# Optimization experiments

Measured on AMD Instinct MI355X. Metric: run time of the kernel, lower is better.

Reference implementation:

```python
import jax, jax.numpy as jnp
import numpy as np

B, N, K, D, H, W = 16, 32, 32, 64, 128, 128  # batch, instances, dot_number, dot_dimension, fmap HxW
IMAGE_SIZE = 512.0
DOWN = 4.0
HID = 128


def setup_inputs() -> dict:
    key = jax.random.key(0)
    ks = jax.random.split(key, 16)
    s = 0.05
    x = jax.random.normal(ks[0], (B, 64, H, W), jnp.float32)
    mask_point = jax.random.uniform(ks[1], (B, N, K, 2), jnp.float32) * 511.0  # image-space coords
    point_mask = jnp.ones((B, N, K), jnp.int32)  # 1 = real point, 0 = zero-padded
    return {
        "x": x,
        "mask_point": mask_point,
        "point_mask": point_mask,
        "conv1_w": jax.random.normal(ks[2], (64, 64, 3, 3), jnp.float32) * s,
        "conv1_b": jnp.zeros((64,), jnp.float32),
        "conv2_w": jax.random.normal(ks[3], (D, 64), jnp.float32) * s,
        "conv2_b": jnp.full((D,), -2.19, jnp.float32),  # bias_fill with bias_value
        "Wih_e": jax.random.normal(ks[4], (4 * HID, D), jnp.float32) * s,
        "Whh_e": jax.random.normal(ks[5], (4 * HID, HID), jnp.float32) * s,
        "bih_e": jnp.zeros((4 * HID,), jnp.float32),
        "bhh_e": jnp.zeros((4 * HID,), jnp.float32),
        "Wih_d": jax.random.normal(ks[6], (4 * HID, HID), jnp.float32) * s,
        "Whh_d": jax.random.normal(ks[7], (4 * HID, HID), jnp.float32) * s,
        "bih_d": jnp.zeros((4 * HID,), jnp.float32),
        "bhh_d": jnp.zeros((4 * HID,), jnp.float32),
        "W1": jax.random.normal(ks[8], (64, HID), jnp.float32) * s,
        "b1": jnp.zeros((64,), jnp.float32),
        "W2": jax.random.normal(ks[9], (2, 64), jnp.float32) * s,
        "b2": jnp.zeros((2,), jnp.float32),
    }


def _lstm(seq, Wih, Whh, bih, bhh, h0, c0):
    # seq: [T, Bflat, in]; PyTorch gate order i, f, g, o
    bias = bih + bhh
    def step(carry, xt):
        h, c = carry
        g = xt @ Wih.T + h @ Whh.T + bias
        i, f, gg, o = jnp.split(g, 4, axis=-1)
        c = jax.nn.sigmoid(f) * c + jax.nn.sigmoid(i) * jnp.tanh(gg)
        h = jax.nn.sigmoid(o) * jnp.tanh(c)
        return (h, c), h
    (hT, cT), ys = jax.lax.scan(step, (h0, c0), seq)
    return ys, (hT, cT)


def reference(x, mask_point, point_mask, conv1_w, conv1_b, conv2_w, conv2_b,
              Wih_e, Whh_e, bih_e, bhh_e, Wih_d, Whh_d, bih_d, bhh_d,
              W1, b1, W2, b2):
    # SingleHead extraction: 3x3 conv -> ReLU -> 1x1 conv
    feat = jax.lax.conv_general_dilated(
        x, conv1_w, (1, 1), 'SAME',
        dimension_numbers=('NCHW', 'OIHW', 'NCHW')) + conv1_b[None, :, None, None]
    feat = jax.nn.relu(feat)
    fmap = jnp.einsum('bchw,dc->bdhw', feat, conv2_w) + conv2_b[None, :, None, None]
    xf = fmap.reshape(B, D, H * W)

    # keypoint index math (vectorized version of the nested python loops)
    pts = jnp.minimum(mask_point / DOWN, 127.0)        # [B,N,K,2] feature-map coords
    gt = pts * DOWN                                     # gt_keypoints
    flat = (pts[..., 1] * (IMAGE_SIZE / DOWN) + pts[..., 0]).astype(jnp.int32)  # [B,N,K]

    # gather dot features; zero padding where point_mask == 0
    dots = jax.vmap(lambda f, idx: f.T[idx])(xf, flat)  # [B,N,K,D]
    dots = dots * point_mask[..., None].astype(dots.dtype)

    seq = dots.reshape(B * N, K, D).transpose(1, 0, 2)  # [K, B*N, D] (time-major)
    h0 = jnp.zeros((B * N, HID), seq.dtype)
    enc, (h, c) = _lstm(seq, Wih_e, Whh_e, bih_e, bhh_e, h0, h0)
    dec, _ = _lstm(enc, Wih_d, Whh_d, bih_d, bhh_d, h, c)

    y = jax.nn.relu(dec @ W1.T + b1) @ W2.T + b2        # [K, B*N, 2]
    kp = y.transpose(1, 0, 2).reshape(B, N, K, 2)
    return kp, gt
```

## Files before the change

kernel.cpp:

```cpp
#include <hip/hip_runtime.h>
#include <stdint.h>

#define NSEQ 512
#define HIDN 128

#define OFF_FEIH   0
#define OFF_BIAS_E 65536
#define OFF_BIAS_D 67584
#define OFF_W1P    69632
#define OFF_W2P    143360
#define OFF_FLAT   151552
#define OFF_W1H    217088
#define OFF_FEHH   233472
#define OFF_FDIH8  364544
#define OFF_FDHH8  430080
#define OFF_W2T    495616
#define OFF_DOTS   (1024*1024)
#define OFF_XT     (4*1024*1024)
#define WS_NEED_XT ((size_t)(4*1024*1024) + (size_t)16*128*128*64*2 + 1024)

typedef _Float16 h2f __attribute__((ext_vector_type(2)));
typedef _Float16 f16x8 __attribute__((ext_vector_type(8)));
typedef float    f32x4 __attribute__((ext_vector_type(4)));

static __device__ __forceinline__ h2f u2h(uint32_t u) {
  union { uint32_t u; h2f h; } v; v.u = u; return v.h;
}

#if __has_builtin(__builtin_amdgcn_fdot2)
static __device__ __forceinline__ float fdot2_(uint32_t a, uint32_t b, float c) {
  return __builtin_amdgcn_fdot2(u2h(a), u2h(b), c, false);
}
#else
static __device__ __forceinline__ float fdot2_(uint32_t a, uint32_t b, float c) {
  h2f x = u2h(a), y = u2h(b);
  return c + (float)x.x * (float)y.x + (float)x.y * (float)y.y;
}
#endif

static __device__ __forceinline__ uint32_t packh(float a, float b) {
  union { _Float16 h[2]; uint32_t u; } v;
  v.h[0] = (_Float16)a; v.h[1] = (_Float16)b; return v.u;
}
static __device__ __forceinline__ float sig_(float x) {
  return 1.0f / (1.0f + __expf(-x));
}
static __device__ __forceinline__ float tanh_(float x) {
  return 1.0f - 2.0f / (1.0f + __expf(2.0f * x));
}

static __device__ __forceinline__ uint32_t f2e4m3_sw(float f) {
  union { float f; uint32_t u; } v; v.f = f;
  uint32_t s = (v.u >> 24) & 0x80u;
  float af = fabsf(f);
  if (af == 0.0f) return s;
  if (af >= 448.0f) return s | 0x7Eu;
  int e; float m = frexpf(af, &e);
  int E = e + 6;
  float mant = m * 2.0f - 1.0f;
  int mm = (int)(mant * 8.0f + 0.5f);
  if (mm == 8) { mm = 0; ++E; }
  if (E < 1) {
    int sm = (int)(af * 512.0f + 0.5f);
    return s | (uint32_t)(sm > 7 ? 7 : sm);
  }
  if (E > 15) return s | 0x7Eu;
  return s | ((uint32_t)E << 3) | (uint32_t)mm;
}
static __device__ __forceinline__ uint32_t pk4_fp8(float a, float b, float c, float d) {
#if __has_builtin(__builtin_amdgcn_cvt_pk_fp8_f32)
  int r = __builtin_amdgcn_cvt_pk_fp8_f32(a, b, 0, false);
  r = __builtin_amdgcn_cvt_pk_fp8_f32(c, d, r, true);
  return (uint32_t)r;
#else
  return f2e4m3_sw(a) | (f2e4m3_sw(b) << 8) | (f2e4m3_sw(c) << 16) | (f2e4m3_sw(d) << 24);
#endif
}
static __device__ __forceinline__ uint8_t f8_(float v) {
#if __has_builtin(__builtin_amdgcn_cvt_pk_fp8_f32)
  return (uint8_t)(__builtin_amdgcn_cvt_pk_fp8_f32(v, 0.f, 0, false) & 0xFF);
#else
  return (uint8_t)f2e4m3_sw(v);
#endif
}
static __device__ __forceinline__ long u2l(uint2 v) {
  union { uint2 v; long l; } x; x.v = v; return x.l;
}
static __device__ __forceinline__ uint2 ldg_frag8(const uint2* p) {
  uint2 r;
  asm volatile("global_load_dwordx2 %0, %1, off" : "=v"(r) : "v"(p));
  return r;
}
static __device__ __forceinline__ void frag_fence() {
  asm volatile("s_waitcnt vmcnt(0)" ::: "memory");
  __builtin_amdgcn_sched_barrier(0);
}

__global__ __launch_bounds__(256) void prep_kernel(
    const float* Wih_e, const float* Whh_e,
    const float* bih_e, const float* bhh_e,
    const float* Wih_d, const float* Whh_d,
    const float* bih_d, const float* bhh_d,
    const float* w1, const float* w2, const float* W1,
    const float* mask_point, float* out_gt, int* flat,
    char* ws, int w1_order) {
  float*    bias_e = (float*)(ws + OFF_BIAS_E);
  float*    bias_d = (float*)(ws + OFF_BIAS_D);
  uint32_t* w1p    = (uint32_t*)(ws + OFF_W1P);
  uint32_t* w2p    = (uint32_t*)(ws + OFF_W2P);
  uint32_t* W1h    = (uint32_t*)(ws + OFF_W1H);
  uint32_t* w2t    = (uint32_t*)(ws + OFF_W2T);

  int idx = blockIdx.x * 256 + threadIdx.x;
  if (idx < 16384) {
    int j2 = idx & 3, lane = (idx >> 2) & 63, kt = (idx >> 8) & 1, gt = idx >> 9;
    int g = gt*16 + (lane & 15);
    int k = kt*32 + ((lane >> 4) & 3)*8 + 2*j2;
    ((uint32_t*)(ws + OFF_FEIH))[idx] = packh(Wih_e[g*64 + k], Wih_e[g*64 + k + 1]);
    return;
  }
  idx -= 16384;
  if (idx < 512) { bias_e[idx] = bih_e[idx] + bhh_e[idx]; return; }
  idx -= 512;
  if (idx < 512) { bias_d[idx] = bih_d[idx] + bhh_d[idx]; return; }
  idx -= 512;
  if (idx < 288*64) {
    int i2 = idx >> 6, c = idx & 63;
    if (w1_order) {
      int tap = i2 >> 5, cin = (i2 & 31) * 2;
      w1p[idx] = packh(w1[c*576 + cin*9 + tap], w1[c*576 + (cin+1)*9 + tap]);
    } else {
      w1p[idx] = packh(w1[c*576 + 2*i2], w1[c*576 + 2*i2 + 1]);
    }
    return;
  }
  idx -= 288*64;
  if (idx < 32*64) {
    int c2 = idx >> 6, d = idx & 63;
    w2p[idx] = packh(w2[d*64 + 2*c2], w2[d*64 + 2*c2 + 1]);
    return;
  }
  idx -= 32*64;
  if (idx < 64*64) {
    int k2 = idx >> 6, j = idx & 63;
    W1h[idx] = packh(W1[j*128 + 2*k2], W1[j*128 + 2*k2 + 1]);
    return;
  }
  idx -= 64*64;
  if (idx < 32768) {
    int j2 = idx & 3, lane = (idx >> 2) & 63, kt = (idx >> 8) & 3, gt = idx >> 10;
    int g = gt*16 + (lane & 15);
    int k = kt*32 + ((lane >> 4) & 3)*8 + 2*j2;
    ((uint32_t*)(ws + OFF_FEHH))[idx] = packh(Whh_e[g*128 + k], Whh_e[g*128 + k + 1]);
    return;
  }
  idx -= 32768;
  if (idx < 16384) {
    int half = idx & 1, lane = (idx >> 1) & 63, kt = (idx >> 7) & 3, gt = idx >> 9;
    int g = gt*16 + (lane & 15);
    int kb = kt*32 + ((lane >> 4) & 3)*8 + half*4;
    const float* W = Wih_d;
    ((uint32_t*)(ws + OFF_FDIH8))[(((gt*4 + kt)*64 + lane) << 1) | half] =
        pk4_fp8(W[g*128 + kb], W[g*128 + kb + 1], W[g*128 + kb + 2], W[g*128 + kb + 3]);
    return;
  }
  idx -= 16384;
  if (idx < 16384) {
    int half = idx & 1, lane = (idx >> 1) & 63, kt = (idx >> 7) & 3, gt = idx >> 9;
    int g = gt*16 + (lane & 15);
    int kb = kt*32 + ((lane >> 4) & 3)*8 + half*4;
    const float* W = Whh_d;
    ((uint32_t*)(ws + OFF_FDHH8))[(((gt*4 + kt)*64 + lane) << 1) | half] =
        pk4_fp8(W[g*128 + kb], W[g*128 + kb + 1], W[g*128 + kb + 2], W[g*128 + kb + 3]);
    return;
  }
  idx -= 16384;
  if (idx < 64*36) {
    int d = idx / 36, c2 = idx - (idx/36)*36;
    w2t[idx] = (c2 < 32) ? packh(w2[d*64 + 2*c2], w2[d*64 + 2*c2 + 1]) : 0u;
    return;
  }
  idx -= 64*36;
  if (idx < 16384) {
    float mx = mask_point[idx*2 + 0];
    float my = mask_point[idx*2 + 1];
    float fx = fminf(mx * 0.25f, 127.0f);
    float fy = fminf(my * 0.25f, 127.0f);
    out_gt[idx*2 + 0] = fx * 4.0f;
    out_gt[idx*2 + 1] = fy * 4.0f;
    flat[idx] = (int)(__fmaf_rn(fy, 128.0f, fx));
    return;
  }
}
#define PREP_TOTAL (16384 + 512 + 512 + 288*64 + 32*64 + 64*64 + 32768 + 16384 + 16384 + 64*36 + 16384)

__global__ __launch_bounds__(256, 2) void transpose_kernel(
    const float* x, uint32_t* xT32) {
  __shared__ float lds[64][257];
  int bid = blockIdx.x;
  int xt = bid & 3, yt = (bid >> 2) & 15, b = bid >> 6;
  int x0 = xt * 32, y0 = yt * 8;
  int tx = threadIdx.x & 31, ty = threadIdx.x >> 5;
  #pragma unroll 8
  for (int c = 0; c < 64; ++c)
    lds[c][ty*32 + tx] = x[((b*64 + c)*128 + (y0 + ty))*128 + (x0 + tx)];
  __syncthreads();
  #pragma unroll 8
  for (int r = 0; r < 32; ++r) {
    int i = threadIdx.x + 256*r;
    int c2 = i & 31, pos = i >> 5;
    int yy = pos >> 5, xx = pos & 31;
    float lo = lds[2*c2][yy*32 + xx], hi = lds[2*c2 + 1][yy*32 + xx];
    xT32[((b*128 + y0 + yy)*128 + (x0 + xx))*32 + c2] = packh(lo, hi);
  }
}

__global__ __launch_bounds__(512, 1) void conv_mfma_kernel(
    const uint32_t* xT32, const int* point_mask,
    const float* conv1_b, const float* conv2_b,
    const char* ws_ro, _Float16* dots_h, const int* flat) {
  __shared__ __attribute__((aligned(16))) uint32_t w1s[64*292];
  __shared__ __attribute__((aligned(16))) uint32_t patch2[32*292];
  __shared__ __attribute__((aligned(16))) uint32_t t1s[32*36];

  const uint32_t* w1p = (const uint32_t*)(ws_ro + OFF_W1P);
  const uint32_t* w2t = (const uint32_t*)(ws_ro + OFF_W2T);
  int tid  = threadIdx.x;
  int lane = tid & 63, wave = tid >> 6;
  int r = wave & 3, g = wave >> 2;
  int cl = lane & 15, lgrp = lane >> 4;

  for (int i = tid; i < 288*64; i += 512) {
    int i2 = i >> 6, cc = i & 63;
    w1s[cc*292 + i2] = w1p[i];
  }

  uint4 a2[2];
  #pragma unroll
  for (int kt = 0; kt < 2; ++kt)
    a2[kt] = *(const uint4*)&w2t[(r*16 + cl)*36 + kt*16 + lgrp*4];

  float4 b1v = *(const float4*)&conv1_b[r*16 + lgrp*4];
  float4 b2v = *(const float4*)&conv2_b[r*16 + lgrp*4];

  for (int it = 0; it < 2; ++it) {
    int p0 = blockIdx.x * 64 + it * 32;
    __syncthreads();
    #pragma unroll
    for (int rr = 0; rr < 18; ++rr) {
      int u = tid + 512*rr;
      int slot = u / 288, w = u - slot*288;
      int tap = w >> 5, c2i = w & 31;
      int p = p0 + slot;
      int fl = flat[p];
      int hh = fl >> 7, ww = fl & 127;
      int b = p >> 10;
      int dy = tap / 3, dx = tap - dy*3;
      int yy = hh + dy - 1, xx = ww + dx - 1;
      uint32_t v = 0u;
      if (yy >= 0 && yy < 128 && xx >= 0 && xx < 128)
        v = xT32[((b*128 + yy)*128 + xx)*32 + c2i];
      patch2[slot*292 + w] = v;
    }
    __syncthreads();

    f32x4 acc = {b1v.x, b1v.y, b1v.z, b1v.w};
    #pragma unroll
    for (int kt = 0; kt < 18; ++kt) {
      f16x8 af = *(const f16x8*)&w1s[(r*16 + cl)*292 + kt*16 + lgrp*4];
      f16x8 bf = *(const f16x8*)&patch2[(g*16 + cl)*292 + kt*16 + lgrp*4];
      acc = __builtin_amdgcn_mfma_f32_16x16x32_f16(af, bf, acc, 0, 0, 0);
    }
    {
      int trow = (g*16 + cl)*36 + r*8 + lgrp*2;
      t1s[trow]     = packh(fmaxf(acc[0], 0.f), fmaxf(acc[1], 0.f));
      t1s[trow + 1] = packh(fmaxf(acc[2], 0.f), fmaxf(acc[3], 0.f));
    }
    __syncthreads();

    f32x4 acc2 = {b2v.x, b2v.y, b2v.z, b2v.w};
    #pragma unroll
    for (int kt = 0; kt < 2; ++kt) {
      f16x8 af; __builtin_memcpy(&af, &a2[kt], 16);
      f16x8 bf = *(const f16x8*)&t1s[(g*16 + cl)*36 + kt*16 + lgrp*4];
      acc2 = __builtin_amdgcn_mfma_f32_16x16x32_f16(af, bf, acc2, 0, 0, 0);
    }
    {
      int p = p0 + g*16 + cl;
      float m = (float)point_mask[p];
      int kk = p & 31, bn = p >> 5;
      int d0 = r*16 + lgrp*4;
      uint2 o;
      o.x = packh(acc2[0]*m, acc2[1]*m);
      o.y = packh(acc2[2]*m, acc2[3]*m);
      *(uint2*)&dots_h[(size_t)(kk*NSEQ + bn)*64 + d0] = o;
    }
  }
}

__global__ __launch_bounds__(256, 2) void conv_gather_kernel(
    const float* x, const int* point_mask,
    const float* conv1_b, const float* conv2_b,
    const char* ws_ro, _Float16* dots_h, const int* flat) {
  __shared__ uint32_t w1s[64*292];
  __shared__ uint32_t patch2[4*288];
  __shared__ uint32_t tl2[4*32];

  const uint32_t* w1p = (const uint32_t*)(ws_ro + OFF_W1P);
  const uint32_t* w2p = (const uint32_t*)(ws_ro + OFF_W2P);
  int tid = threadIdx.x;
  for (int i = tid; i < 288*64; i += 256) {
    int i2 = i >> 6, cc = i & 63;
    w1s[cc*292 + i2] = w1p[i];
  }

  int q = tid >> 6, c = tid & 63;
  float c1b = conv1_b[c], c2b = conv2_b[c];

  for (int g = 0; g < 8; ++g) {
    int p0 = blockIdx.x * 32 + g * 4;
    __syncthreads();
    #pragma unroll
    for (int r = 0; r < 9; ++r) {
      int l = tid + 256*r;
      int slot = l / 576;
      int within = l - slot*576;
      int cp = within / 9;
      int tap = within - cp*9;
      int p = p0 + slot;
      int fl = flat[p];
      int hh = fl >> 7, ww = fl & 127;
      int b = p >> 10;
      int yy = hh + tap/3 - 1, xx = ww + tap%3 - 1;
      float v = 0.0f;
      if (yy >= 0 && yy < 128 && xx >= 0 && xx < 128)
        v = x[((b*64 + cp)*128 + yy)*128 + xx];
      ((_Float16*)patch2)[l] = (_Float16)v;
    }
    __syncthreads();

    float a0 = c1b, a1 = 0.f, a2 = 0.f, a3 = 0.f;
    int cbase = c * 292, pbase = q * 288;
    #pragma unroll 4
    for (int i2 = 0; i2 < 288; i2 += 4) {
      a0 = fdot2_(w1s[cbase + i2+0], patch2[pbase + i2+0], a0);
      a1 = fdot2_(w1s[cbase + i2+1], patch2[pbase + i2+1], a1);
      a2 = fdot2_(w1s[cbase + i2+2], patch2[pbase + i2+2], a2);
      a3 = fdot2_(w1s[cbase + i2+3], patch2[pbase + i2+3], a3);
    }
    float t1 = fmaxf((a0 + a1) + (a2 + a3), 0.0f);
    ((_Float16*)tl2)[q*64 + c] = (_Float16)t1;

    float acc2 = c2b;
    #pragma unroll
    for (int c2i = 0; c2i < 32; ++c2i)
      acc2 = fdot2_(w2p[c2i*64 + c], tl2[q*32 + c2i], acc2);
    int p = p0 + q;
    acc2 *= (float)point_mask[p];
    int k = p & 31, bn = p >> 5;
    dots_h[(k*NSEQ + bn)*64 + c] = (_Float16)acc2;
  }
}

__global__ __launch_bounds__(512, 2) void lstm_head_kernel(
    const char* ws_ro,
    const float* b1, const float* W2, const float* b2,
    float* out_kp) {
  const f16x8* feih   = (const f16x8*)(ws_ro + OFF_FEIH);
  const f16x8* fehh   = (const f16x8*)(ws_ro + OFF_FEHH);
  const uint2* fdih8  = (const uint2*)(ws_ro + OFF_FDIH8);
  const uint2* fdhh8  = (const uint2*)(ws_ro + OFF_FDHH8);
  const float* bias_e = (const float*)(ws_ro + OFF_BIAS_E);
  const float* bias_d = (const float*)(ws_ro + OFF_BIAS_D);
  const uint32_t* dots_u = (const uint32_t*)(ws_ro + OFF_DOTS);
  const uint32_t* W1h = (const uint32_t*)(ws_ro + OFF_W1H);

  __shared__ __attribute__((aligned(16))) uint32_t xs[2][32][32];
  __shared__ __attribute__((aligned(16))) uint32_t enc8[2][32][32];
  __shared__ __attribute__((aligned(16))) uint32_t dech2[2][32][64];
  __shared__ __attribute__((aligned(16))) uint32_t hb2[2][64];
  __shared__ __attribute__((aligned(16))) uint32_t hb8[2][32];
  __shared__ __attribute__((aligned(16))) float    gb[2][512];
  __shared__ float hidf[64][65];

  int tid  = threadIdx.x;
  int lane = tid & 63, wave = tid >> 6;
  int col  = lane & 15, lgrp = lane >> 4;
  int sb   = col & 1;
  int bn0  = blockIdx.x * 2;

  int s_nl = tid >> 7, u_nl = tid & 127;
  float c_reg = 0.0f;

  for (int i = tid; i < 2048; i += 512) {
    int s = i >> 10, rem = i & 1023, t = rem >> 5, k2 = rem & 31;
    xs[s][t][k2] = dots_u[(t*NSEQ + bn0 + s)*32 + k2];
  }

  f16x8 ax[4][2], ae[4][4];
  #pragma unroll
  for (int g0 = 0; g0 < 4; ++g0) {
    #pragma unroll
    for (int kt = 0; kt < 2; ++kt)
      ax[g0][kt] = feih[((wave*4 + g0)*2 + kt)*64 + lane];
    #pragma unroll
    for (int kt = 0; kt < 4; ++kt)
      ae[g0][kt] = fehh[((wave*4 + g0)*4 + kt)*64 + lane];
  }

  float be0 = bias_e[u_nl],       be1 = bias_e[128 + u_nl];
  float be2 = bias_e[256 + u_nl], be3 = bias_e[384 + u_nl];

  if (tid < 128) hb2[tid >> 6][tid & 63] = 0u;
  __syncthreads();

  const f16x8 bzero = {};

  for (int t = 0; t < 32; ++t) {
    f16x8 bx[2], bf[4];
    #pragma unroll
    for (int kt = 0; kt < 2; ++kt)
      bx[kt] = *(const f16x8*)&xs[sb][t][kt*16 + lgrp*4];
    #pragma unroll
    for (int kt = 0; kt < 4; ++kt) {
      if (col < 2) bf[kt] = *(const f16x8*)&hb2[col][kt*16 + lgrp*4];
      else         bf[kt] = bzero;
    }
    #pragma unroll
    for (int g0 = 0; g0 < 4; ++g0) {
      f32x4 acc = {0.f, 0.f, 0.f, 0.f};
      #pragma unroll
      for (int kt = 0; kt < 2; ++kt)
        acc = __builtin_amdgcn_mfma_f32_16x16x32_f16(ax[g0][kt], bx[kt], acc, 0, 0, 0);
      #pragma unroll
      for (int kt = 0; kt < 4; ++kt)
        acc = __builtin_amdgcn_mfma_f32_16x16x32_f16(ae[g0][kt], bf[kt], acc, 0, 0, 0);
      if (col < 2)
        *(f32x4*)&gb[col][(wave*4 + g0)*16 + lgrp*4] = acc;
    }
    __syncthreads();
    if (tid < 256) {
      float ig = sig_ (gb[s_nl][u_nl]       + be0);
      float fg = sig_ (gb[s_nl][128 + u_nl] + be1);
      float gg = tanh_(gb[s_nl][256 + u_nl] + be2);
      float og = sig_ (gb[s_nl][384 + u_nl] + be3);
      c_reg = fg * c_reg + ig * gg;
      float hh = og * tanh_(c_reg);
      ((_Float16*)&hb2[s_nl][0])[u_nl] = (_Float16)hh;
      ((uint8_t*)&enc8[s_nl][t][0])[u_nl] = f8_(hh);
    }
    __syncthreads();
  }

  if (tid < 256) {
    float hv = (float)((_Float16*)&hb2[s_nl][0])[u_nl];
    ((uint8_t*)&hb8[s_nl][0])[u_nl] = f8_(hv);
  }

  uint2 dih8[4][4], dhh8[4][4];
  #pragma unroll
  for (int g0 = 0; g0 < 4; ++g0)
    #pragma unroll
    for (int kt = 0; kt < 4; ++kt) {
      dih8[g0][kt] = ldg_frag8(&fdih8[((wave*4 + g0)*4 + kt)*64 + lane]);
      dhh8[g0][kt] = ldg_frag8(&fdhh8[((wave*4 + g0)*4 + kt)*64 + lane]);
    }
  frag_fence();
  float bdi = 0.f, bdf = 0.f, bdg = 0.f, bdo = 0.f;
  if (tid < 256) {
    bdi = bias_d[u_nl];       bdf = bias_d[128 + u_nl];
    bdg = bias_d[256 + u_nl]; bdo = bias_d[384 + u_nl];
  }
  __syncthreads();

  for (int t = 0; t < 32; ++t) {
    long bx[4], bh[4];
    #pragma unroll
    for (int kt = 0; kt < 4; ++kt) {
      if (col < 2) {
        bx[kt] = u2l(*(const uint2*)&enc8[col][t][kt*8 + lgrp*2]);
        bh[kt] = u2l(*(const uint2*)&hb8[col][kt*8 + lgrp*2]);
      } else { bx[kt] = 0; bh[kt] = 0; }
    }
    #pragma unroll
    for (int g0 = 0; g0 < 4; ++g0) {
      f32x4 acc = {0.f, 0.f, 0.f, 0.f};
      #pragma unroll
      for (int kt = 0; kt < 4; ++kt)
        acc = __builtin_amdgcn_mfma_f32_16x16x32_fp8_fp8(
            u2l(dih8[g0][kt]), bx[kt], acc, 0, 0, 0);
      #pragma unroll
      for (int kt = 0; kt < 4; ++kt)
        acc = __builtin_amdgcn_mfma_f32_16x16x32_fp8_fp8(
            u2l(dhh8[g0][kt]), bh[kt], acc, 0, 0, 0);
      if (col < 2)
        *(f32x4*)&gb[col][(wave*4 + g0)*16 + lgrp*4] = acc;
    }
    __syncthreads();
    if (tid < 256) {
      float ig = sig_ (gb[s_nl][u_nl]       + bdi);
      float fg = sig_ (gb[s_nl][128 + u_nl] + bdf);
      float gg = tanh_(gb[s_nl][256 + u_nl] + bdg);
      float og = sig_ (gb[s_nl][384 + u_nl] + bdo);
      c_reg = fg * c_reg + ig * gg;
      float hh = og * tanh_(c_reg);
      ((uint8_t*)&hb8[s_nl][0])[u_nl] = f8_(hh);
      ((_Float16*)&dech2[s_nl][t][0])[u_nl] = (_Float16)hh;
    }
    __syncthreads();
  }

  {
    int j = tid & 63, w = tid >> 6;
    float acc[8];
    #pragma unroll
    for (int m = 0; m < 8; ++m) acc[m] = b1[j];
    #pragma unroll 8
    for (int k = 0; k < 64; ++k) {
      uint32_t wv = W1h[k*64 + j];
      #pragma unroll
      for (int m = 0; m < 8; ++m) {
        int st = w + 8*m;
        acc[m] = fdot2_(wv, dech2[st >> 5][st & 31][k], acc[m]);
      }
    }
    #pragma unroll
    for (int m = 0; m < 8; ++m) {
      int st = w + 8*m;
      hidf[st][j] = fmaxf(acc[m], 0.0f);
    }
  }
  __syncthreads();
  if (tid < 128) {
    int st = tid >> 1, e = tid & 1;
    float acc = b2[e];
    #pragma unroll 16
    for (int j = 0; j < 64; ++j) acc += W2[e*64 + j] * hidf[st][j];
    int s = st >> 5, t = st & 31;
    out_kp[((bn0 + s)*32 + t)*2 + e] = acc;
  }
}

extern "C" void kernel_launch(void* const* d_in, const int* in_sizes, int n_in,
                              void* d_out, int out_size, void* d_ws, size_t ws_size,
                              hipStream_t stream) {
  const float* x          = (const float*)d_in[0];
  const float* mask_point = (const float*)d_in[1];
  const int*   point_mask = (const int*)d_in[2];
  const float* conv1_w    = (const float*)d_in[3];
  const float* conv1_b    = (const float*)d_in[4];
  const float* conv2_w    = (const float*)d_in[5];
  const float* conv2_b    = (const float*)d_in[6];
  const float* Wih_e      = (const float*)d_in[7];
  const float* Whh_e      = (const float*)d_in[8];
  const float* bih_e      = (const float*)d_in[9];
  const float* bhh_e      = (const float*)d_in[10];
  const float* Wih_d      = (const float*)d_in[11];
  const float* Whh_d      = (const float*)d_in[12];
  const float* bih_d      = (const float*)d_in[13];
  const float* bhh_d      = (const float*)d_in[14];
  const float* W1         = (const float*)d_in[15];
  const float* b1         = (const float*)d_in[16];
  const float* W2         = (const float*)d_in[17];
  const float* b2         = (const float*)d_in[18];

  float* out = (float*)d_out;
  char*  ws  = (char*)d_ws;

  const bool use_xt = (ws_size >= WS_NEED_XT);

  prep_kernel<<<(PREP_TOTAL + 255)/256, 256, 0, stream>>>(
      Wih_e, Whh_e, bih_e, bhh_e, Wih_d, Whh_d, bih_d, bhh_d,
      conv1_w, conv2_w, W1, mask_point, out + 32768, (int*)(ws + OFF_FLAT),
      ws, use_xt ? 1 : 0);

  if (use_xt) {
    transpose_kernel<<<1024, 256, 0, stream>>>(x, (uint32_t*)(ws + OFF_XT));
    conv_mfma_kernel<<<256, 512, 0, stream>>>(
        (const uint32_t*)(ws + OFF_XT), point_mask, conv1_b, conv2_b,
        ws, (_Float16*)(ws + OFF_DOTS), (const int*)(ws + OFF_FLAT));
  } else {
    conv_gather_kernel<<<512, 256, 0, stream>>>(
        x, point_mask, conv1_b, conv2_b,
        ws, (_Float16*)(ws + OFF_DOTS), (const int*)(ws + OFF_FLAT));
  }

  lstm_head_kernel<<<256, 512, 0, stream>>>(ws, b1, W2, b2, out);
}
```

Before: 121.3 us.

## Store transposed input in FP8 and run conv1 with FP8 MFMA, fuse prep launch

The channel-last copy of the input is now stored as FP8 (e4m3) instead of FP16, which halves the bytes written by the transpose and read by the gather. The 3x3 conv weights are prepacked as FP8 scaled by 16, and conv1 uses the fp8 16x16x32 MFMA, with the result rescaled after ReLU. The prep kernel is merged into the transpose launch as extra blocks, which removes one kernel launch. The cost is lower input precision in conv1, a possible accuracy problem, plus a changed workspace requirement.

```diff
diff --git a/kernel.cpp b/kernel.cpp
--- a/kernel.cpp
+++ b/kernel.cpp
@@ -15,9 +15,10 @@
 #define OFF_FDIH8  364544
 #define OFF_FDHH8  430080
 #define OFF_W2T    495616
+#define OFF_W1F8   504832
 #define OFF_DOTS   (1024*1024)
 #define OFF_XT     (4*1024*1024)
-#define WS_NEED_XT ((size_t)(4*1024*1024) + (size_t)16*128*128*64*2 + 1024)
+#define WS_NEED_XT ((size_t)(4*1024*1024) + (size_t)16*128*128*64 + 1024)
 
 typedef _Float16 h2f __attribute__((ext_vector_type(2)));
 typedef _Float16 f16x8 __attribute__((ext_vector_type(8)));
@@ -96,7 +97,7 @@
   __builtin_amdgcn_sched_barrier(0);
 }
 
-__global__ __launch_bounds__(256) void prep_kernel(
+static __device__ void prep_body(int idx,
     const float* Wih_e, const float* Whh_e,
     const float* bih_e, const float* bhh_e,
     const float* Wih_d, const float* Whh_d,
@@ -110,8 +111,8 @@
   uint32_t* w2p    = (uint32_t*)(ws + OFF_W2P);
   uint32_t* W1h    = (uint32_t*)(ws + OFF_W1H);
   uint32_t* w2t    = (uint32_t*)(ws + OFF_W2T);
-
-  int idx = blockIdx.x * 256 + threadIdx.x;
+  uint32_t* w1f8   = (uint32_t*)(ws + OFF_W1F8);
+
   if (idx < 16384) {
     int j2 = idx & 3, lane = (idx >> 2) & 63, kt = (idx >> 8) & 1, gt = idx >> 9;
     int g = gt*16 + (lane & 15);
@@ -181,6 +182,16 @@
     return;
   }
   idx -= 64*36;
+  if (idx < 64*144) {
+    int c = idx / 144, j = idx - (idx/144)*144;
+    int tap = j >> 4, cin0 = (j & 15) * 4;
+    w1f8[idx] = pk4_fp8(w1[c*576 + (cin0+0)*9 + tap] * 16.0f,
+                        w1[c*576 + (cin0+1)*9 + tap] * 16.0f,
+                        w1[c*576 + (cin0+2)*9 + tap] * 16.0f,
+                        w1[c*576 + (cin0+3)*9 + tap] * 16.0f);
+    return;
+  }
+  idx -= 64*144;
   if (idx < 16384) {
     float mx = mask_point[idx*2 + 0];
     float my = mask_point[idx*2 + 1];
@@ -192,12 +203,33 @@
     return;
   }
 }
-#define PREP_TOTAL (16384 + 512 + 512 + 288*64 + 32*64 + 64*64 + 32768 + 16384 + 16384 + 64*36 + 16384)
-
-__global__ __launch_bounds__(256, 2) void transpose_kernel(
-    const float* x, uint32_t* xT32) {
+#define PREP_TOTAL (16384 + 512 + 512 + 288*64 + 32*64 + 64*64 + 32768 + 16384 + 16384 + 64*36 + 64*144 + 16384)
+#define PREP_BLOCKS ((PREP_TOTAL + 255) / 256)
+
+__global__ __launch_bounds__(256) void prep_kernel(
+    const float* Wih_e, const float* Whh_e, const float* bih_e, const float* bhh_e,
+    const float* Wih_d, const float* Whh_d, const float* bih_d, const float* bhh_d,
+    const float* w1, const float* w2, const float* W1,
+    const float* mask_point, float* out_gt, int* flat, char* ws, int w1_order) {
+  prep_body(blockIdx.x * 256 + threadIdx.x,
+            Wih_e, Whh_e, bih_e, bhh_e, Wih_d, Whh_d, bih_d, bhh_d,
+            w1, w2, W1, mask_point, out_gt, flat, ws, w1_order);
+}
+
+__global__ __launch_bounds__(256, 2) void transpose_prep_kernel(
+    const float* x, uint32_t* xT8,
+    const float* Wih_e, const float* Whh_e, const float* bih_e, const float* bhh_e,
+    const float* Wih_d, const float* Whh_d, const float* bih_d, const float* bhh_d,
+    const float* w1, const float* w2, const float* W1,
+    const float* mask_point, float* out_gt, int* flat, char* ws) {
   __shared__ float lds[64][257];
   int bid = blockIdx.x;
+  if (bid >= 1024) {
+    prep_body((bid - 1024) * 256 + threadIdx.x,
+              Wih_e, Whh_e, bih_e, bhh_e, Wih_d, Whh_d, bih_d, bhh_d,
+              w1, w2, W1, mask_point, out_gt, flat, ws, 1);
+    return;
+  }
   int xt = bid & 3, yt = (bid >> 2) & 15, b = bid >> 6;
   int x0 = xt * 32, y0 = yt * 8;
   int tx = threadIdx.x & 31, ty = threadIdx.x >> 5;
@@ -206,33 +238,35 @@
     lds[c][ty*32 + tx] = x[((b*64 + c)*128 + (y0 + ty))*128 + (x0 + tx)];
   __syncthreads();
   #pragma unroll 8
-  for (int r = 0; r < 32; ++r) {
+  for (int r = 0; r < 16; ++r) {
     int i = threadIdx.x + 256*r;
-    int c2 = i & 31, pos = i >> 5;
+    int c4 = i & 15, pos = i >> 4;
     int yy = pos >> 5, xx = pos & 31;
-    float lo = lds[2*c2][yy*32 + xx], hi = lds[2*c2 + 1][yy*32 + xx];
-    xT32[((b*128 + y0 + yy)*128 + (x0 + xx))*32 + c2] = packh(lo, hi);
-  }
-}
-
-__global__ __launch_bounds__(512, 1) void conv_mfma_kernel(
-    const uint32_t* xT32, const int* point_mask,
+    uint32_t v = pk4_fp8(lds[c4*4+0][pos], lds[c4*4+1][pos],
+                         lds[c4*4+2][pos], lds[c4*4+3][pos]);
+    xT8[((b*128 + y0 + yy)*128 + (x0 + xx))*16 + c4] = v;
+  }
+}
+
+__global__ __launch_bounds__(512, 2) void conv_mfma8_kernel(
+    const uint32_t* xT8, const int* point_mask,
     const float* conv1_b, const float* conv2_b,
     const char* ws_ro, _Float16* dots_h, const int* flat) {
-  __shared__ __attribute__((aligned(16))) uint32_t w1s[64*292];
-  __shared__ __attribute__((aligned(16))) uint32_t patch2[32*292];
+  __shared__ __attribute__((aligned(16))) uint32_t w1s8[64*146];
+  __shared__ __attribute__((aligned(16))) uint32_t patch8[32*146];
   __shared__ __attribute__((aligned(16))) uint32_t t1s[32*36];
 
-  const uint32_t* w1p = (const uint32_t*)(ws_ro + OFF_W1P);
-  const uint32_t* w2t = (const uint32_t*)(ws_ro + OFF_W2T);
+  const uint32_t* w1f8 = (const uint32_t*)(ws_ro + OFF_W1F8);
+  const uint32_t* w2t  = (const uint32_t*)(ws_ro + OFF_W2T);
   int tid  = threadIdx.x;
   int lane = tid & 63, wave = tid >> 6;
   int r = wave & 3, g = wave >> 2;
   int cl = lane & 15, lgrp = lane >> 4;
 
-  for (int i = tid; i < 288*64; i += 512) {
-    int i2 = i >> 6, cc = i & 63;
-    w1s[cc*292 + i2] = w1p[i];
+  #pragma unroll
+  for (int i = tid; i < 64*144; i += 512) {
+    int c = i / 144, j = i - c*144;
+    w1s8[c*146 + j] = w1f8[i];
   }
 
   uint4 a2[2];
@@ -240,17 +274,18 @@
   for (int kt = 0; kt < 2; ++kt)
     a2[kt] = *(const uint4*)&w2t[(r*16 + cl)*36 + kt*16 + lgrp*4];
 
-  float4 b1v = *(const float4*)&conv1_b[r*16 + lgrp*4];
+  float4 b1r = *(const float4*)&conv1_b[r*16 + lgrp*4];
   float4 b2v = *(const float4*)&conv2_b[r*16 + lgrp*4];
+  f32x4 b1v = {b1r.x*16.f, b1r.y*16.f, b1r.z*16.f, b1r.w*16.f};
 
   for (int it = 0; it < 2; ++it) {
     int p0 = blockIdx.x * 64 + it * 32;
     __syncthreads();
     #pragma unroll
-    for (int rr = 0; rr < 18; ++rr) {
+    for (int rr = 0; rr < 9; ++rr) {
       int u = tid + 512*rr;
-      int slot = u / 288, w = u - slot*288;
-      int tap = w >> 5, c2i = w & 31;
+      int slot = u / 144, j = u - slot*144;
+      int tap = j >> 4, c4 = j & 15;
       int p = p0 + slot;
       int fl = flat[p];
       int hh = fl >> 7, ww = fl & 127;
@@ -259,22 +294,22 @@
       int yy = hh + dy - 1, xx = ww + dx - 1;
       uint32_t v = 0u;
       if (yy >= 0 && yy < 128 && xx >= 0 && xx < 128)
-        v = xT32[((b*128 + yy)*128 + xx)*32 + c2i];
-      patch2[slot*292 + w] = v;
-    }
-    __syncthreads();
-
-    f32x4 acc = {b1v.x, b1v.y, b1v.z, b1v.w};
+        v = xT8[((b*128 + yy)*128 + xx)*16 + c4];
+      patch8[slot*146 + j] = v;
+    }
+    __syncthreads();
+
+    f32x4 acc = b1v;
     #pragma unroll
     for (int kt = 0; kt < 18; ++kt) {
-      f16x8 af = *(const f16x8*)&w1s[(r*16 + cl)*292 + kt*16 + lgrp*4];
-      f16x8 bf = *(const f16x8*)&patch2[(g*16 + cl)*292 + kt*16 + lgrp*4];
-      acc = __builtin_amdgcn_mfma_f32_16x16x32_f16(af, bf, acc, 0, 0, 0);
+      long af = u2l(*(const uint2*)&w1s8[(r*16 + cl)*146 + kt*8 + lgrp*2]);
+      long bf = u2l(*(const uint2*)&patch8[(g*16 + cl)*146 + kt*8 + lgrp*2]);
+      acc = __builtin_amdgcn_mfma_f32_16x16x32_fp8_fp8(af, bf, acc, 0, 0, 0);
     }
     {
       int trow = (g*16 + cl)*36 + r*8 + lgrp*2;
-      t1s[trow]     = packh(fmaxf(acc[0], 0.f), fmaxf(acc[1], 0.f));
-      t1s[trow + 1] = packh(fmaxf(acc[2], 0.f), fmaxf(acc[3], 0.f));
+      t1s[trow]     = packh(fmaxf(acc[0], 0.f) * 0.0625f, fmaxf(acc[1], 0.f) * 0.0625f);
+      t1s[trow + 1] = packh(fmaxf(acc[2], 0.f) * 0.0625f, fmaxf(acc[3], 0.f) * 0.0625f);
     }
     __syncthreads();
 
@@ -569,17 +604,19 @@
 
   const bool use_xt = (ws_size >= WS_NEED_XT);
 
-  prep_kernel<<<(PREP_TOTAL + 255)/256, 256, 0, stream>>>(
-      Wih_e, Whh_e, bih_e, bhh_e, Wih_d, Whh_d, bih_d, bhh_d,
-      conv1_w, conv2_w, W1, mask_point, out + 32768, (int*)(ws + OFF_FLAT),
-      ws, use_xt ? 1 : 0);
-
   if (use_xt) {
-    transpose_kernel<<<1024, 256, 0, stream>>>(x, (uint32_t*)(ws + OFF_XT));
-    conv_mfma_kernel<<<256, 512, 0, stream>>>(
+    transpose_prep_kernel<<<1024 + PREP_BLOCKS, 256, 0, stream>>>(
+        x, (uint32_t*)(ws + OFF_XT),
+        Wih_e, Whh_e, bih_e, bhh_e, Wih_d, Whh_d, bih_d, bhh_d,
+        conv1_w, conv2_w, W1, mask_point, out + 32768, (int*)(ws + OFF_FLAT), ws);
+    conv_mfma8_kernel<<<256, 512, 0, stream>>>(
         (const uint32_t*)(ws + OFF_XT), point_mask, conv1_b, conv2_b,
         ws, (_Float16*)(ws + OFF_DOTS), (const int*)(ws + OFF_FLAT));
   } else {
+    prep_kernel<<<PREP_BLOCKS, 256, 0, stream>>>(
+        Wih_e, Whh_e, bih_e, bhh_e, Wih_d, Whh_d, bih_d, bhh_d,
+        conv1_w, conv2_w, W1, mask_point, out + 32768, (int*)(ws + OFF_FLAT),
+        ws, 1);
     conv_gather_kernel<<<512, 256, 0, stream>>>(
         x, point_mask, conv1_b, conv2_b,
         ws, (_Float16*)(ws + OFF_DOTS), (const int*)(ws + OFF_FLAT));
```

Result: faster. 106.1 us (-12.6%).
